# Optimization experiments

Measured on AMD Instinct MI355X. Metric: run time of the kernel, lower is better.

The kernel has to match this reference:

```python
import jax, jax.numpy as jnp
import numpy as np

SIG = [1, 1, 1, 1, -1]  # Cl(4,1)
NVEC = 5
GA = 1 << NVEC  # 32


def _build_gp_table():
    # Cayley table for the geometric product on blades indexed by bitmask.
    G = np.zeros((GA, GA, GA), np.float32)
    for a in range(GA):
        for b in range(GA):
            s = 0
            t = a >> 1
            while t:
                s += bin(t & b).count('1')
                t >>= 1
            sign = -1.0 if (s & 1) else 1.0
            common = a & b
            for i in range(NVEC):
                if (common >> i) & 1:
                    sign *= SIG[i]
            G[a, b, a ^ b] = sign
    return G

GP_TABLE = jnp.asarray(_build_gp_table())


def geometric_product(x, y):
    return jnp.einsum('...i,...j,ijk->...k', x, y, GP_TABLE)


def manifold_norm(x):
    # normalize each multivector onto the unit sphere in R^32
    return x / (jnp.linalg.norm(x, axis=-1, keepdims=True) + 1e-6)


def versor_linear(x, W, b):
    # channel mixing shared across multivector components: x [..., in, ga]
    return jnp.einsum('...ig,oi->...og', x, W) + b


def layer_norm2d(x, w, b):
    # LayerNorm over last two dims [D, ga] jointly
    mu = jnp.mean(x, axis=(-2, -1), keepdims=True)
    var = jnp.var(x, axis=(-2, -1), keepdims=True)
    return (x - mu) / jnp.sqrt(var + 1e-5) * w + b


def attention(x, Wq, bq, Wk, bk, Wv, bv, Wo, bo, n_heads):
    B, S, D, G = x.shape
    dh = D // n_heads
    q = versor_linear(x, Wq, bq).reshape(B, S, n_heads, dh, G)
    k = versor_linear(x, Wk, bk).reshape(B, S, n_heads, dh, G)
    v = versor_linear(x, Wv, bv).reshape(B, S, n_heads, dh, G)
    scale = 1.0 / np.sqrt(dh * G).astype(np.float32)
    scores = jnp.einsum('bshdg,bthdg->bhst', q, k) * scale
    probs = jax.nn.softmax(scores, axis=-1)
    o = jnp.einsum('bhst,bthdg->bshdg', probs, v).reshape(B, S, D, G)
    return versor_linear(o, Wo, bo)


N_HEADS = 8


def forward(x, Wq, bq, Wk, bk, Wv, bv, Wo, bo, ln1_w, ln1_b, ln2_w, ln2_b,
            gamma1, gamma2, W1, b1, W2, b2, Wr, br, Wc, bc):
    L = Wq.shape[0]
    for l in range(L):
        h = attention(layer_norm2d(x, ln1_w[l], ln1_b[l]),
                      Wq[l], bq[l], Wk[l], bk[l], Wv[l], bv[l], Wo[l], bo[l], N_HEADS)
        x = manifold_norm(x + gamma1[l] * h)
        m = versor_linear(layer_norm2d(x, ln2_w[l], ln2_b[l]), W1[l], b1[l])
        m = versor_linear(jnp.tanh(m), W2[l], b2[l])
        x = manifold_norm(x + gamma2[l] * m)
    # RecursiveRotorAccumulator: log(S)-step inclusive scan of rotors
    delta = versor_linear(x, Wr, br)
    rot = 0.5 * delta
    rot = rot.at[..., 0].add(1.0)
    rot = manifold_norm(rot)
    S = x.shape[1]
    step = 1
    while step < S:
        left = rot[:, :-step]
        right = rot[:, step:]
        comb = manifold_norm(geometric_product(right, left))
        rot = jnp.concatenate([rot[:, :step], comb], axis=1)
        step *= 2
    pooled = rot[:, -1]  # [B, D, ga]
    logits = pooled.reshape(pooled.shape[0], -1) @ Wc.T + bc
    return logits


def setup_inputs() -> dict:
    key = jax.random.key(0)
    B, S, D, G, L, NC = 8, 256, 64, GA, 4, 1000
    E = 4 * D  # expansion hidden
    ks = jax.random.split(key, 16)
    sd = 0.02
    inp = {
        'x': jax.random.normal(ks[0], (B, S, D, G), jnp.float32),
        'Wq': jax.random.normal(ks[1], (L, D, D), jnp.float32) * sd,
        'bq': jnp.zeros((L, D, G), jnp.float32),
        'Wk': jax.random.normal(ks[2], (L, D, D), jnp.float32) * sd,
        'bk': jnp.zeros((L, D, G), jnp.float32),
        'Wv': jax.random.normal(ks[3], (L, D, D), jnp.float32) * sd,
        'bv': jnp.zeros((L, D, G), jnp.float32),
        'Wo': jax.random.normal(ks[4], (L, D, D), jnp.float32) * sd,
        'bo': jnp.zeros((L, D, G), jnp.float32),
        'ln1_w': jnp.ones((L, D, G), jnp.float32),
        'ln1_b': jnp.zeros((L, D, G), jnp.float32),
        'ln2_w': jnp.ones((L, D, G), jnp.float32),
        'ln2_b': jnp.zeros((L, D, G), jnp.float32),
        'gamma1': 1e-5 * jnp.ones((L, D, G), jnp.float32),
        'gamma2': 1e-5 * jnp.ones((L, D, G), jnp.float32),
        'W1': jax.random.normal(ks[5], (L, E, D), jnp.float32) * sd,
        'b1': jnp.zeros((L, E, G), jnp.float32),
        'W2': jax.random.normal(ks[6], (L, D, E), jnp.float32) * sd,
        'b2': jnp.zeros((L, D, G), jnp.float32),
        'Wr': jax.random.normal(ks[7], (D, D), jnp.float32) * sd,
        'br': jnp.zeros((D, G), jnp.float32),
        'Wc': jax.random.normal(ks[8], (NC, D * G), jnp.float32) * sd,
        'bc': jnp.zeros((NC,), jnp.float32),
    }
    return inp


def reference(x, Wq, bq, Wk, bk, Wv, bv, Wo, bo, ln1_w, ln1_b, ln2_w, ln2_b,
              gamma1, gamma2, W1, b1, W2, b2, Wr, br, Wc, bc):
    return forward(x, Wq, bq, Wk, bk, Wv, bv, Wo, bo, ln1_w, ln1_b, ln2_w, ln2_b,
                   gamma1, gamma2, W1, b1, W2, b2, Wr, br, Wc, bc)
```

## Files before the change

kernel.cpp:

```cpp
#include <hip/hip_runtime.h>
#include <hip/hip_bf16.h>

constexpr int kB  = 8;
constexpr int kS  = 256;
constexpr int kD  = 64;
constexpr int kG  = 32;
constexpr int kE  = 256;
constexpr int kNH = 8;
constexpr int kHD = 256;
constexpr int kDG = kD * kG;
constexpr int kT  = kB * kS;
constexpr int kNC = 1000;

using bf16x8 = __attribute__((ext_vector_type(8))) short;
using f32x4  = __attribute__((ext_vector_type(4))) float;

__device__ __forceinline__ short f2bf(float f) {
    unsigned u = __float_as_uint(f);
    unsigned r = (u + 0x7FFFu + ((u >> 16) & 1u)) >> 16;
    return (short)r;
}

__device__ __forceinline__ float tanh_fast(float x) {
    float a = fabsf(x);
    float e = __expf(-2.f * a);
    float d = 1.f + e;
    float r = __builtin_amdgcn_rcpf(d);
    r = r * (2.f - d * r);
    float t = (1.f - e) * r;
    return copysignf(t, x);
}

__global__ __launch_bounds__(256) void cvtw_kernel(
    const float* __restrict__ Wq, const float* __restrict__ Wk,
    const float* __restrict__ Wv, const float* __restrict__ Wo,
    const float* __restrict__ W1, const float* __restrict__ W2,
    unsigned short* __restrict__ dst) {
    int idx = (blockIdx.x * 256 + threadIdx.x) * 4;
    const float* src; int off;
    if      (idx <  16384) { src = Wq; off = 0; }
    else if (idx <  32768) { src = Wk; off = 16384; }
    else if (idx <  49152) { src = Wv; off = 32768; }
    else if (idx <  65536) { src = Wo; off = 49152; }
    else if (idx < 131072) { src = W1; off = 65536; }
    else                   { src = W2; off = 131072; }
    const float4 v = *(const float4*)(src + (idx - off));
    *(short4*)&dst[idx] = make_short4(f2bf(v.x), f2bf(v.y), f2bf(v.z), f2bf(v.w));
}

__global__ __launch_bounds__(256) void prep_tr_kernel(
    const float* __restrict__ bq, const float* __restrict__ bk,
    const float* __restrict__ bv, const float* __restrict__ bo,
    const float* __restrict__ b2, const float* __restrict__ gm1,
    const float* __restrict__ gm2, const float* __restrict__ ln2w,
    const float* __restrict__ ln2b, const float* __restrict__ ln1w,
    const float* __restrict__ ln1b, const float* __restrict__ b1,
    float* __restrict__ dst) {
    __shared__ float lt[32 * 257];
    const int a = blockIdx.x >> 2, l = blockIdx.x & 3;
    const float* srcs[12] = {bq, bk, bv, bo, b2, gm1, gm2, ln2w, ln2b, ln1w, ln1b, b1};
    const int R  = (a == 11) ? 256 : 64;
    const int sh = (a == 11) ? 8 : 6;
    const float* src = srcs[a] + (size_t)l * R * 32;
    float* out = dst + a * 8192 + l * R * 32;
    const int tid = threadIdx.x;
    for (int j = tid; j < R * 32; j += 256) lt[(j & 31) * (R + 1) + (j >> 5)] = src[j];
    __syncthreads();
    for (int k = tid; k < R * 32; k += 256) {
        int g = k >> sh, r = k & (R - 1);
        out[k] = lt[g * (R + 1) + r];
    }
}

__global__ __launch_bounds__(256) void ln_kernel(const float* __restrict__ Xin,
                                                 const float* __restrict__ w,
                                                 const float* __restrict__ b,
                                                 unsigned short* __restrict__ A,
                                                 float* __restrict__ XT) {
    int t = blockIdx.x, tid = threadIdx.x;
    const float* xp = Xin + (size_t)t * kDG;
    __shared__ float r1[256], r2[256];
    __shared__ short st[32 * 72];
    __shared__ float xf[32 * 68];
    float v[8], s = 0.f, ss = 0.f;
#pragma unroll
    for (int j = 0; j < 8; j++) {
        float x = xp[tid + j * 256];
        v[j] = x; s += x; ss += x * x;
        int jj = tid + j * 256;
        xf[(jj & 31) * 68 + (jj >> 5)] = x;
    }
    r1[tid] = s; r2[tid] = ss; __syncthreads();
    for (int o = 128; o > 0; o >>= 1) {
        if (tid < o) { r1[tid] += r1[tid + o]; r2[tid] += r2[tid + o]; }
        __syncthreads();
    }
    float mean = r1[0] * (1.f / kDG);
    float var  = r2[0] * (1.f / kDG) - mean * mean;
    float rstd = rsqrtf(var + 1e-5f);
#pragma unroll
    for (int j = 0; j < 8; j++) {
        int jj = tid + j * 256;
        float val = (v[j] - mean) * rstd * w[jj] + b[jj];
        st[(jj & 31) * 72 + (jj >> 5)] = f2bf(val);
    }
    __syncthreads();
    bf16x8 ov = *(const bf16x8*)&st[(tid >> 3) * 72 + (tid & 7) * 8];
    *(bf16x8*)&A[(size_t)t * kDG + tid * 8] = ov;
    const int row = tid >> 3, col = (tid & 7) * 8;
    float* xo = XT + (size_t)t * kDG + tid * 8;
    *(float4*)(xo + 0) = *(const float4*)&xf[row * 68 + col + 0];
    *(float4*)(xo + 4) = *(const float4*)&xf[row * 68 + col + 4];
}

template<int MT>
__device__ __forceinline__ void epiT(
    const f32x4 (&acc)[MT][2], const float* __restrict__ bT,
    float* __restrict__ XTp, const float* __restrict__ gT,
    int l16, int quad, int obase,
    float& s, float& ss, float (&xv)[MT][2][4]) {
    s = 0.f; ss = 0.f;
#pragma unroll
    for (int mt = 0; mt < MT; ++mt) {
        int o0 = obase + mt * 16 + quad * 4;
        float vv[2][4];
#pragma unroll
        for (int nt = 0; nt < 2; ++nt) {
            int g = nt * 16 + l16;
            const float4 b4 = *(const float4*)&bT[g * kD + o0];
            const float4 g4 = *(const float4*)&gT[g * kD + o0];
            const float4 xi = *(const float4*)&XTp[g * kD + o0];
#pragma unroll
            for (int r = 0; r < 4; ++r)
                vv[nt][r] = (&xi.x)[r] + (&g4.x)[r] * (acc[mt][nt][r] + (&b4.x)[r]);
        }
        float rn[4];
#pragma unroll
        for (int r = 0; r < 4; ++r) {
            float sq = vv[0][r] * vv[0][r] + vv[1][r] * vv[1][r];
#pragma unroll
            for (int off = 1; off < 16; off <<= 1) sq += __shfl_xor(sq, off, 64);
            rn[r] = 1.f / (sqrtf(sq) + 1e-6f);
        }
#pragma unroll
        for (int nt = 0; nt < 2; ++nt) {
            int g = nt * 16 + l16;
            float4 xo;
#pragma unroll
            for (int r = 0; r < 4; ++r) {
                float x = vv[nt][r] * rn[r];
                (&xo.x)[r] = x; xv[mt][nt][r] = x;
                s += x; ss = fmaf(x, x, ss);
            }
            *(float4*)&XTp[g * kD + o0] = xo;
        }
    }
}

template<int MT>
__device__ __forceinline__ void lnT(
    const float (&xv)[MT][2][4], const float* __restrict__ lwT,
    const float* __restrict__ lbT, unsigned short* __restrict__ Aoutp,
    int l16, int quad, int obase, float mean, float rstd) {
#pragma unroll
    for (int mt = 0; mt < MT; ++mt)
#pragma unroll
        for (int nt = 0; nt < 2; ++nt) {
            int g = nt * 16 + l16;
            int o0 = obase + mt * 16 + quad * 4;
            const float4 w4 = *(const float4*)&lwT[g * kD + o0];
            const float4 b4 = *(const float4*)&lbT[g * kD + o0];
            short4 s4;
#pragma unroll
            for (int r = 0; r < 4; ++r)
                (&s4.x)[r] = f2bf((xv[mt][nt][r] - mean) * rstd * (&w4.x)[r] + (&b4.x)[r]);
            *(short4*)&Aoutp[g * kD + o0] = s4;
        }
}

__global__ __launch_bounds__(256) void vlinT_kernel(const float* __restrict__ XT,
                                                    const float* __restrict__ W,
                                                    const float* __restrict__ bias,
                                                    float* __restrict__ OutT) {
    __shared__ float sx[32 * 65];
    __shared__ float sw[kD * kD];
    int t = blockIdx.x, tid = threadIdx.x;
    const float* xp = XT + (size_t)t * kDG;
    for (int j = tid; j < kDG; j += 256) sx[(j >> 6) * 65 + (j & 63)] = xp[j];
    for (int j = tid; j < kD * kD; j += 256) sw[j] = W[j];
    __syncthreads();
    int g = tid & 31, ob = tid >> 5;
    int b = t >> 8, s = t & 255;
    float* op = OutT + ((size_t)b * kD * kS + s) * kG;
    for (int o = ob; o < kD; o += 8) {
        float acc = bias[o * kG + g];
        const float* wr = sw + o * kD;
#pragma unroll
        for (int i = 0; i < kD; i++) acc += wr[i] * sx[g * 65 + i];
        op[(size_t)o * kS * kG + g] = acc;
    }
}

template<bool DO_LN>
__global__ __launch_bounds__(128, 4) void mlp_fused_kernel(
    const unsigned short* __restrict__ A,
    const unsigned short* __restrict__ W1h,
    const float* __restrict__ b1T,
    const unsigned short* __restrict__ W2h,
    const float* __restrict__ b2T,
    float* __restrict__ XT, const float* __restrict__ gmT,
    const float* __restrict__ lwT, const float* __restrict__ lbT,
    unsigned short* __restrict__ Aout) {
    constexpr int MS = 264;
    __shared__ short sM[32 * MS];
    __shared__ float sred[4];
    const int tid = threadIdx.x;
    const int w = tid >> 6, lane = tid & 63;
    const int l16 = lane & 15, quad = lane >> 4;
    const int tok = blockIdx.x;

    const unsigned short* xp = A + (size_t)tok * kDG;
    bf16x8 bfr[2][2];
#pragma unroll
    for (int c = 0; c < 2; ++c)
#pragma unroll
        for (int nt = 0; nt < 2; ++nt)
            bfr[c][nt] = *(const bf16x8*)&xp[(nt * 16 + l16) * kD + c * 32 + quad * 8];

    f32x4 acc[8][2];
#pragma unroll
    for (int mt = 0; mt < 8; ++mt)
#pragma unroll
        for (int nt = 0; nt < 2; ++nt) acc[mt][nt] = (f32x4){0.f, 0.f, 0.f, 0.f};

#pragma unroll
    for (int mt = 0; mt < 8; ++mt)
#pragma unroll
        for (int c = 0; c < 2; ++c) {
            bf16x8 afr = *(const bf16x8*)&W1h[((w * 8 + mt) * 16 + l16) * kD + c * 32 + quad * 8];
#pragma unroll
            for (int nt = 0; nt < 2; ++nt)
                acc[mt][nt] = __builtin_amdgcn_mfma_f32_16x16x32_bf16(afr, bfr[c][nt], acc[mt][nt], 0, 0, 0);
        }

#pragma unroll
    for (int mt = 0; mt < 8; ++mt)
#pragma unroll
        for (int nt = 0; nt < 2; ++nt) {
            int g = nt * 16 + l16;
            int e0 = (w * 8 + mt) * 16 + quad * 4;
            const float4 b4 = *(const float4*)&b1T[g * kE + e0];
            short4 s4;
#pragma unroll
            for (int r = 0; r < 4; ++r)
                (&s4.x)[r] = f2bf(tanh_fast(acc[mt][nt][r] + (&b4.x)[r]));
            *(short4*)&sM[g * MS + e0] = s4;
        }
    __syncthreads();

    f32x4 acc2[2][2];
#pragma unroll
    for (int mt = 0; mt < 2; ++mt)
#pragma unroll
        for (int nt = 0; nt < 2; ++nt) acc2[mt][nt] = (f32x4){0.f, 0.f, 0.f, 0.f};

#pragma unroll
    for (int c = 0; c < 8; ++c) {
        bf16x8 bq[2];
#pragma unroll
        for (int nt = 0; nt < 2; ++nt)
            bq[nt] = *(const bf16x8*)&sM[(nt * 16 + l16) * MS + c * 32 + quad * 8];
#pragma unroll
        for (int mt = 0; mt < 2; ++mt) {
            bf16x8 afr = *(const bf16x8*)&W2h[(w * 32 + mt * 16 + l16) * kE + c * 32 + quad * 8];
#pragma unroll
            for (int nt = 0; nt < 2; ++nt)
                acc2[mt][nt] = __builtin_amdgcn_mfma_f32_16x16x32_bf16(afr, bq[nt], acc2[mt][nt], 0, 0, 0);
        }
    }

    const size_t tb = (size_t)tok * kDG;
    float xv[2][2][4]; float s, ss;
    epiT<2>(acc2, b2T, XT + tb, gmT, l16, quad, w * 32, s, ss, xv);
    if (DO_LN) {
#pragma unroll
        for (int off = 1; off < 64; off <<= 1) {
            s += __shfl_xor(s, off, 64); ss += __shfl_xor(ss, off, 64);
        }
        if (lane == 0) { sred[w] = s; sred[2 + w] = ss; }
        __syncthreads();
        float st = sred[0] + sred[1], sst = sred[2] + sred[3];
        float mean = st * (1.f / kDG);
        float var  = sst * (1.f / kDG) - mean * mean;
        float rstd = rsqrtf(var + 1e-5f);
        lnT<2>(xv, lwT, lbT, Aout + tb, l16, quad, w * 32, mean, rstd);
    }
}

__global__ __launch_bounds__(256, 3) void gemmWo_fused_kernel(
    const unsigned short* __restrict__ X, const unsigned short* __restrict__ Wh,
    const float* __restrict__ bT,
    float* __restrict__ XT, const float* __restrict__ gmT,
    const float* __restrict__ lwT, const float* __restrict__ lbT,
    unsigned short* __restrict__ Aout) {
    constexpr int WS = 64 + 8;
    __shared__ short sW[64 * WS];

    const int tid = threadIdx.x, wave = tid >> 6, lane = tid & 63;
    const int l16 = lane & 15, quad = lane >> 4;
    const int tok = blockIdx.x * 4 + wave;

    for (int j = tid * 8; j < 64 * 64; j += 2048) {
        int o = j >> 6, i = j & 63;
        *(bf16x8*)&sW[o * WS + i] = *(const bf16x8*)(Wh + j);
    }

    const unsigned short* xp = X + (size_t)tok * kDG;
    bf16x8 bfr[2][2];
#pragma unroll
    for (int c = 0; c < 2; ++c)
#pragma unroll
        for (int nt = 0; nt < 2; ++nt)
            bfr[c][nt] = *(const bf16x8*)&xp[(nt * 16 + l16) * kD + c * 32 + quad * 8];
    __syncthreads();

    f32x4 acc[4][2];
#pragma unroll
    for (int mt = 0; mt < 4; ++mt)
#pragma unroll
        for (int nt = 0; nt < 2; ++nt) acc[mt][nt] = (f32x4){0.f, 0.f, 0.f, 0.f};

#pragma unroll
    for (int mt = 0; mt < 4; ++mt)
#pragma unroll
        for (int c = 0; c < 2; ++c) {
            bf16x8 afr = *(const bf16x8*)&sW[(mt * 16 + l16) * WS + c * 32 + quad * 8];
#pragma unroll
            for (int nt = 0; nt < 2; ++nt)
                acc[mt][nt] = __builtin_amdgcn_mfma_f32_16x16x32_bf16(afr, bfr[c][nt], acc[mt][nt], 0, 0, 0);
        }

    const size_t tb = (size_t)tok * kDG;
    float xv[4][2][4]; float s, ss;
    epiT<4>(acc, bT, XT + tb, gmT, l16, quad, 0, s, ss, xv);
#pragma unroll
    for (int off = 1; off < 64; off <<= 1) {
        s += __shfl_xor(s, off, 64); ss += __shfl_xor(ss, off, 64);
    }
    float mean = s * (1.f / kDG);
    float var  = ss * (1.f / kDG) - mean * mean;
    float rstd = rsqrtf(var + 1e-5f);
    lnT<4>(xv, lwT, lbT, Aout + tb, l16, quad, 0, mean, rstd);
}

__global__ __launch_bounds__(256, 3) void gemm_qkv_kernel(
    const unsigned short* __restrict__ X,
    const unsigned short* __restrict__ Wqh, const unsigned short* __restrict__ Wkh,
    const unsigned short* __restrict__ Wvh,
    const float* __restrict__ bqT, const float* __restrict__ bkT, const float* __restrict__ bvT,
    unsigned short* __restrict__ Q, unsigned short* __restrict__ K, unsigned short* __restrict__ V) {
    constexpr int WS = 64 + 8;
    __shared__ short sW[3 * 64 * WS];

    const int tid = threadIdx.x, wave = tid >> 6, lane = tid & 63;
    const int l16 = lane & 15, quad = lane >> 4;
    const int tok = blockIdx.x * 4 + wave;

    const unsigned short* Wp[3] = {Wqh, Wkh, Wvh};
#pragma unroll
    for (int w = 0; w < 3; ++w)
        for (int j = tid * 8; j < 64 * 64; j += 2048) {
            int o = j >> 6, i = j & 63;
            *(bf16x8*)&sW[w * 64 * WS + o * WS + i] = *(const bf16x8*)(Wp[w] + j);
        }

    const unsigned short* xp = X + (size_t)tok * kDG;
    bf16x8 bfr[2][2];
#pragma unroll
    for (int c = 0; c < 2; ++c)
#pragma unroll
        for (int nt = 0; nt < 2; ++nt)
            bfr[c][nt] = *(const bf16x8*)&xp[(nt * 16 + l16) * kD + c * 32 + quad * 8];
    __syncthreads();

    f32x4 acc[3][4][2];
#pragma unroll
    for (int w = 0; w < 3; ++w)
#pragma unroll
        for (int mt = 0; mt < 4; ++mt)
#pragma unroll
            for (int nt = 0; nt < 2; ++nt) acc[w][mt][nt] = (f32x4){0.f, 0.f, 0.f, 0.f};

#pragma unroll
    for (int w = 0; w < 3; ++w)
#pragma unroll
        for (int mt = 0; mt < 4; ++mt)
#pragma unroll
            for (int c = 0; c < 2; ++c) {
                bf16x8 afr = *(const bf16x8*)&sW[w * 64 * WS + (mt * 16 + l16) * WS + c * 32 + quad * 8];
#pragma unroll
                for (int nt = 0; nt < 2; ++nt)
                    acc[w][mt][nt] = __builtin_amdgcn_mfma_f32_16x16x32_bf16(afr, bfr[c][nt], acc[w][mt][nt], 0, 0, 0);
            }

    unsigned short* Op[3] = {Q, K, V};
    const float* Bp[3] = {bqT, bkT, bvT};
#pragma unroll
    for (int w = 0; w < 3; ++w) {
        unsigned short* op = Op[w] + (size_t)tok * kDG;
#pragma unroll
        for (int mt = 0; mt < 4; ++mt)
#pragma unroll
            for (int nt = 0; nt < 2; ++nt) {
                int g = nt * 16 + l16;
                int o0 = mt * 16 + quad * 4;
                const float4 b4 = *(const float4*)&Bp[w][g * kD + o0];
#pragma unroll
                for (int r = 0; r < 4; ++r)
                    op[(o0 + r) * kG + g] = (unsigned short)f2bf(acc[w][mt][nt][r] + (&b4.x)[r]);
            }
    }
}

constexpr int QSTR = 264;
constexpr int VSTR = 40;

__global__ __launch_bounds__(256) void attn_mfma_kernel(const unsigned short* __restrict__ Q,
                                                        const unsigned short* __restrict__ K,
                                                        const unsigned short* __restrict__ V,
                                                        unsigned short* __restrict__ O) {
    __shared__ short sQ[64 * QSTR];
    __shared__ short sKV[2][256 * VSTR];

    const int qt = blockIdx.x, h = blockIdx.y, b = blockIdx.z;
    const int tid = threadIdx.x;
    const int wave = tid >> 6, lane = tid & 63;
    const int l16 = lane & 15, quad = lane >> 4;

    const size_t bh = (size_t)b * kS * kDG + (size_t)h * kHD;

#pragma unroll
    for (int it = 0; it < 8; ++it) {
        int j = it * 2048 + tid * 8;
        int row = j >> 8, col = j & 255;
        *(bf16x8*)&sQ[row * QSTR + col] =
            *(const bf16x8*)(Q + bh + (size_t)(qt * 64 + row) * kDG + col);
    }
#pragma unroll
    for (int it = 0; it < 4; ++it) {
        int j = it * 2048 + tid * 8;
        int row = j >> 8, col = j & 255;
        *(bf16x8*)&sKV[0][row * QSTR + col] =
            *(const bf16x8*)(K + bh + (size_t)row * kDG + col);
    }
    __syncthreads();

    bf16x8 afrag[8];
    {
        int row = wave * 16 + l16;
#pragma unroll
        for (int c = 0; c < 8; ++c)
            afrag[c] = *(const bf16x8*)&sQ[row * QSTR + c * 32 + quad * 8];
    }

    f32x4 acc[16];
#pragma unroll
    for (int i = 0; i < 16; ++i) acc[i] = (f32x4){0.f, 0.f, 0.f, 0.f};

    for (int kt = 0; kt < 8; ++kt) {
        bf16x8 kpre[4];
        if (kt < 7) {
#pragma unroll
            for (int it = 0; it < 4; ++it) {
                int j = it * 2048 + tid * 8;
                int row = j >> 8, col = j & 255;
                kpre[it] = *(const bf16x8*)(K + bh + (size_t)((kt + 1) * 32 + row) * kDG + col);
            }
        }
        const short* kb = sKV[kt & 1];
#pragma unroll
        for (int nt = 0; nt < 2; ++nt) {
            int key = nt * 16 + l16;
            f32x4 a = acc[kt * 2 + nt];
#pragma unroll
            for (int c = 0; c < 8; ++c) {
                bf16x8 bfrag = *(const bf16x8*)&kb[key * QSTR + c * 32 + quad * 8];
                a = __builtin_amdgcn_mfma_f32_16x16x32_bf16(afrag[c], bfrag, a, 0, 0, 0);
            }
            acc[kt * 2 + nt] = a;
        }
        if (kt < 7) {
            short* nb = sKV[(kt + 1) & 1];
#pragma unroll
            for (int it = 0; it < 4; ++it) {
                int j = it * 2048 + tid * 8;
                int row = j >> 8, col = j & 255;
                *(bf16x8*)&nb[row * QSTR + col] = kpre[it];
            }
            __syncthreads();
        }
    }

    float inv[4];
#pragma unroll
    for (int r = 0; r < 4; ++r) {
        float m = -1e30f;
#pragma unroll
        for (int t = 0; t < 16; ++t) m = fmaxf(m, acc[t][r]);
#pragma unroll
        for (int off = 1; off < 16; off <<= 1) m = fmaxf(m, __shfl_xor(m, off, 16));
        float s = 0.f;
#pragma unroll
        for (int t = 0; t < 16; ++t) {
            float p = __expf((acc[t][r] - m) * 0.0625f);
            acc[t][r] = p; s += p;
        }
#pragma unroll
        for (int off = 1; off < 16; off <<= 1) s += __shfl_xor(s, off, 16);
        inv[r] = 1.f / s;
    }

#pragma unroll
    for (int t = 0; t < 16; ++t)
#pragma unroll
        for (int r = 0; r < 4; ++r)
            sQ[(wave * 16 + quad * 4 + r) * QSTR + t * 16 + l16] = f2bf(acc[t][r]);

    {
        int kb = tid >> 5;
#pragma unroll
        for (int it = 0; it < 2; ++it) {
            int db = (tid & 31) + it * 32;
            short4 vr[4];
#pragma unroll
            for (int r = 0; r < 4; ++r)
                vr[r] = *(const short4*)(V + bh + (size_t)(kb * 4 + r) * kDG + db * 4);
#pragma unroll
            for (int i = 0; i < 4; ++i) {
                short4 p = make_short4((&vr[0].x)[i], (&vr[1].x)[i],
                                       (&vr[2].x)[i], (&vr[3].x)[i]);
                *(short4*)&sKV[0][(db * 4 + i) * VSTR + kb * 4] = p;
            }
        }
    }
    __syncthreads();

    f32x4 oacc[16];
#pragma unroll
    for (int i = 0; i < 16; ++i) oacc[i] = (f32x4){0.f, 0.f, 0.f, 0.f};

    for (int vt = 0; vt < 8; ++vt) {
        short4 vpre[8];
        if (vt < 7) {
            int kb = tid >> 5;
#pragma unroll
            for (int it = 0; it < 2; ++it) {
                int db = (tid & 31) + it * 32;
#pragma unroll
                for (int r = 0; r < 4; ++r)
                    vpre[it * 4 + r] = *(const short4*)(V + bh + (size_t)((vt + 1) * 32 + kb * 4 + r) * kDG + db * 4);
            }
        }
        const short* vb = sKV[vt & 1];
        bf16x8 pfrag = *(const bf16x8*)&sQ[(wave * 16 + l16) * QSTR + vt * 32 + quad * 8];
#pragma unroll
        for (int dt = 0; dt < 16; ++dt) {
            bf16x8 vfrag = *(const bf16x8*)&vb[(dt * 16 + l16) * VSTR + quad * 8];
            oacc[dt] = __builtin_amdgcn_mfma_f32_16x16x32_bf16(pfrag, vfrag, oacc[dt], 0, 0, 0);
        }
        if (vt < 7) {
            short* nb = sKV[(vt + 1) & 1];
            int kb = tid >> 5;
#pragma unroll
            for (int it = 0; it < 2; ++it) {
                int db = (tid & 31) + it * 32;
#pragma unroll
                for (int i = 0; i < 4; ++i) {
                    short4 p = make_short4((&vpre[it * 4 + 0].x)[i], (&vpre[it * 4 + 1].x)[i],
                                           (&vpre[it * 4 + 2].x)[i], (&vpre[it * 4 + 3].x)[i]);
                    *(short4*)&nb[(db * 4 + i) * VSTR + kb * 4] = p;
                }
            }
            __syncthreads();
        }
    }

    {
        const size_t ob = (size_t)(b * kS + qt * 64 + wave * 16 + quad * 4) * kDG + h * 8;
#pragma unroll
        for (int gg = 0; gg < 2; ++gg) {
            int g = gg * 16 + l16;
#pragma unroll
            for (int r = 0; r < 4; ++r) {
                bf16x8 pk;
#pragma unroll
                for (int k = 0; k < 8; ++k)
                    pk[k] = f2bf(oacc[k * 2 + gg][r] * inv[r]);
                *(bf16x8*)&O[ob + (size_t)r * kDG + g * kD] = pk;
            }
        }
    }
}

constexpr int pc_ce(unsigned v) { int c = 0; while (v) { c += v & 1; v >>= 1; } return c; }
constexpr unsigned gp_mask_ce(int a) {
    unsigned m = 0;
    for (int c = 0; c < 32; ++c) {
        int b = a ^ c;
        int s = (a & b) >> 4;
        for (int t = a >> 1; t; t >>= 1) s += pc_ce(t & b);
        if (s & 1) m |= (1u << c);
    }
    return m;
}

template<int A>
__device__ __forceinline__ void gp_term(const float* x, const float* y, float* acc) {
    constexpr unsigned m = gp_mask_ce(A);
    const float xa = x[A], nxa = -xa;
#pragma unroll
    for (int c = 0; c < 32; ++c)
        acc[c] = fmaf(((m >> c) & 1u) ? nxa : xa, y[A ^ c], acc[c]);
}

__device__ __forceinline__ void gp_mn_t(const float* x, const float* y, float* out) {
    float acc[32];
#pragma unroll
    for (int c = 0; c < 32; ++c) acc[c] = 0.f;
    gp_term<0>(x, y, acc);  gp_term<1>(x, y, acc);  gp_term<2>(x, y, acc);  gp_term<3>(x, y, acc);
    gp_term<4>(x, y, acc);  gp_term<5>(x, y, acc);  gp_term<6>(x, y, acc);  gp_term<7>(x, y, acc);
    gp_term<8>(x, y, acc);  gp_term<9>(x, y, acc);  gp_term<10>(x, y, acc); gp_term<11>(x, y, acc);
    gp_term<12>(x, y, acc); gp_term<13>(x, y, acc); gp_term<14>(x, y, acc); gp_term<15>(x, y, acc);
    gp_term<16>(x, y, acc); gp_term<17>(x, y, acc); gp_term<18>(x, y, acc); gp_term<19>(x, y, acc);
    gp_term<20>(x, y, acc); gp_term<21>(x, y, acc); gp_term<22>(x, y, acc); gp_term<23>(x, y, acc);
    gp_term<24>(x, y, acc); gp_term<25>(x, y, acc); gp_term<26>(x, y, acc); gp_term<27>(x, y, acc);
    gp_term<28>(x, y, acc); gp_term<29>(x, y, acc); gp_term<30>(x, y, acc); gp_term<31>(x, y, acc);
    float ss = 0.f;
#pragma unroll
    for (int c = 0; c < 32; ++c) ss = fmaf(acc[c], acc[c], ss);
    float r = 1.f / (sqrtf(ss) + 1e-6f);
#pragma unroll
    for (int c = 0; c < 32; ++c) out[c] = acc[c] * r;
}

__device__ __forceinline__ void leaf_load(const float* base, float* v) {
#pragma unroll
    for (int i = 0; i < 8; ++i) {
        const float4 f = *(const float4*)(base + i * 4);
        v[i * 4 + 0] = 0.5f * f.x; v[i * 4 + 1] = 0.5f * f.y;
        v[i * 4 + 2] = 0.5f * f.z; v[i * 4 + 3] = 0.5f * f.w;
    }
    v[0] += 1.f;
    float ss = 0.f;
#pragma unroll
    for (int c = 0; c < 32; ++c) ss = fmaf(v[c], v[c], ss);
    float r = 1.f / (sqrtf(ss) + 1e-6f);
#pragma unroll
    for (int c = 0; c < 32; ++c) v[c] *= r;
}

__global__ __launch_bounds__(256) void scanreg_kernel(const float* __restrict__ DT,
                                                      float* __restrict__ pooled) {
    const int wave = threadIdx.x >> 6, lane = threadIdx.x & 63;
    const int seq = blockIdx.x * 4 + wave;
    const float* base = DT + ((size_t)seq * kS + lane * 4) * kG;

    float R[32], Y[32], P[32], Xa[32], Yb[32];

    leaf_load(base, R);
    for (int j = 1; j < 4; ++j) {
        leaf_load(base + j * kG, Y);
        gp_mn_t(Y, R, R);
    }

    for (int step = 1; step < 64; step <<= 1) {
        const bool up = lane & step;
#pragma unroll
        for (int c = 0; c < 32; ++c) P[c] = __shfl_xor(R[c], step, 64);
#pragma unroll
        for (int c = 0; c < 32; ++c) {
            Xa[c] = up ? R[c] : P[c];
            Yb[c] = up ? P[c] : R[c];
        }
        gp_mn_t(Xa, Yb, R);
    }

    if (lane == 0) {
        float* op = pooled + (size_t)seq * kG;
#pragma unroll
        for (int i = 0; i < 8; ++i)
            *(float4*)(op + i * 4) = make_float4(R[i * 4], R[i * 4 + 1], R[i * 4 + 2], R[i * 4 + 3]);
    }
}

__global__ __launch_bounds__(256) void cls2_kernel(const float* __restrict__ P,
                                                   const float* __restrict__ Wc,
                                                   const float* __restrict__ bc,
                                                   float* __restrict__ out) {
    __shared__ float sp[kB * kDG];
    const int tid = threadIdx.x, wave = tid >> 6, lane = tid & 63;
    for (int j = tid * 4; j < kB * kDG; j += 1024)
        *(float4*)&sp[j] = *(const float4*)(P + j);
    __syncthreads();

    const int c = blockIdx.x * 4 + wave;
    const float* w = Wc + (size_t)c * kDG;
    float acc[kB];
#pragma unroll
    for (int b = 0; b < kB; ++b) acc[b] = 0.f;
#pragma unroll
    for (int cc = 0; cc < 8; ++cc) {
        const float4 w4 = *(const float4*)(w + cc * 256 + lane * 4);
#pragma unroll
        for (int b = 0; b < kB; ++b) {
            const float4 p4 = *(const float4*)&sp[b * kDG + cc * 256 + lane * 4];
            acc[b] += w4.x * p4.x + w4.y * p4.y + w4.z * p4.z + w4.w * p4.w;
        }
    }
#pragma unroll
    for (int b = 0; b < kB; ++b)
#pragma unroll
        for (int off = 32; off > 0; off >>= 1) acc[b] += __shfl_xor(acc[b], off, 64);
    if (lane == 0) {
        float bias = bc[c];
#pragma unroll
        for (int b = 0; b < kB; ++b) out[b * kNC + c] = acc[b] + bias;
    }
}

extern "C" void kernel_launch(void* const* d_in, const int* in_sizes, int n_in,
                              void* d_out, int out_size, void* d_ws, size_t ws_size,
                              hipStream_t stream) {
    const float* x_in = (const float*)d_in[0];
    const float* Wq   = (const float*)d_in[1];
    const float* bq   = (const float*)d_in[2];
    const float* Wk   = (const float*)d_in[3];
    const float* bk   = (const float*)d_in[4];
    const float* Wv   = (const float*)d_in[5];
    const float* bv   = (const float*)d_in[6];
    const float* Wo   = (const float*)d_in[7];
    const float* bo   = (const float*)d_in[8];
    const float* ln1w = (const float*)d_in[9];
    const float* ln1b = (const float*)d_in[10];
    const float* ln2w = (const float*)d_in[11];
    const float* ln2b = (const float*)d_in[12];
    const float* gm1  = (const float*)d_in[13];
    const float* gm2  = (const float*)d_in[14];
    const float* W1   = (const float*)d_in[15];
    const float* b1   = (const float*)d_in[16];
    const float* W2   = (const float*)d_in[17];
    const float* b2   = (const float*)d_in[18];
    const float* Wr   = (const float*)d_in[19];
    const float* br   = (const float*)d_in[20];
    const float* Wc   = (const float*)d_in[21];
    const float* bc   = (const float*)d_in[22];

    const size_t NEL = (size_t)kT * kDG;
    float* F  = (float*)d_ws;
    float* XT = F;
    unsigned short* Abf = (unsigned short*)(F + NEL);
    unsigned short* Qh = (unsigned short*)(F + 2 * NEL);
    unsigned short* Kh = (unsigned short*)(F + 3 * NEL);
    unsigned short* Vh = (unsigned short*)(F + 4 * NEL);
    unsigned short* Wb = (unsigned short*)(F + 5 * NEL);
    float* PT = F + 3 * NEL + NEL / 2;
    float* pooled = F + 2 * NEL;
    float* DT = F + NEL;

    cvtw_kernel<<<192, 256, 0, stream>>>(Wq, Wk, Wv, Wo, W1, W2, Wb);
    prep_tr_kernel<<<48, 256, 0, stream>>>(bq, bk, bv, bo, b2, gm1, gm2,
                                           ln2w, ln2b, ln1w, ln1b, b1, PT);
    unsigned short* Wqh = Wb;
    unsigned short* Wkh = Wb + 16384;
    unsigned short* Wvh = Wb + 32768;
    unsigned short* Woh = Wb + 49152;
    unsigned short* W1h = Wb + 65536;
    unsigned short* W2h = Wb + 131072;

    auto bqT   = [&](int l) { return PT + 0     + l * 2048; };
    auto bkT   = [&](int l) { return PT + 8192  + l * 2048; };
    auto bvT   = [&](int l) { return PT + 16384 + l * 2048; };
    auto boT   = [&](int l) { return PT + 24576 + l * 2048; };
    auto b2T   = [&](int l) { return PT + 32768 + l * 2048; };
    auto gm1T  = [&](int l) { return PT + 40960 + l * 2048; };
    auto gm2T  = [&](int l) { return PT + 49152 + l * 2048; };
    auto ln2wT = [&](int l) { return PT + 57344 + l * 2048; };
    auto ln2bT = [&](int l) { return PT + 65536 + l * 2048; };
    auto ln1wT = [&](int l) { return PT + 73728 + l * 2048; };
    auto ln1bT = [&](int l) { return PT + 81920 + l * 2048; };
    auto b1T   = [&](int l) { return PT + 90112 + l * 8192; };

    ln_kernel<<<kT, 256, 0, stream>>>(x_in, ln1w, ln1b, Abf, XT);

    for (int l = 0; l < 4; l++) {
        gemm_qkv_kernel<<<kT / 4, 256, 0, stream>>>(Abf,
            Wqh + l * 4096, Wkh + l * 4096, Wvh + l * 4096,
            bqT(l), bkT(l), bvT(l), Qh, Kh, Vh);
        attn_mfma_kernel<<<dim3(4, kNH, kB), 256, 0, stream>>>(Qh, Kh, Vh, Abf);
        gemmWo_fused_kernel<<<kT / 4, 256, 0, stream>>>(Abf, Woh + l * 4096, boT(l),
            XT, gm1T(l), ln2wT(l), ln2bT(l), Abf);
        if (l < 3)
            mlp_fused_kernel<true><<<kT, 128, 0, stream>>>(Abf,
                W1h + l * 16384, b1T(l), W2h + l * 16384, b2T(l),
                XT, gm2T(l), ln1wT(l + 1), ln1bT(l + 1), Abf);
        else
            mlp_fused_kernel<false><<<kT, 128, 0, stream>>>(Abf,
                W1h + l * 16384, b1T(l), W2h + l * 16384, b2T(l),
                XT, gm2T(l), nullptr, nullptr, nullptr);
    }

    vlinT_kernel<<<kT, 256, 0, stream>>>(XT, Wr, br, DT);
    scanreg_kernel<<<kB * kD / 4, 256, 0, stream>>>(DT, pooled);
    cls2_kernel<<<kNC / 4, 256, 0, stream>>>(pooled, Wc, bc, (float*)d_out);
}
```

Baseline: 552.8 us.

## Fuse Wo projection, MLP, and next-layer QKV into one per-token kernel

Merges the Wo GEMM with its residual/normalize/LN2 epilogue, the MLP, and the next layer's LN1 plus QKV projection into a single per-token kernel. Intermediate activations stay in registers and shared memory instead of going through global memory. This removes two kernel launches per layer and the associated global reads and writes. In exchange, Wo and QKV weights are now read directly from global/L2 per block rather than staged in shared memory, and QKV stores are scattered 2-byte writes, which may raise register pressure and store traffic.

```diff
diff --git a/kernel.cpp b/kernel.cpp
--- a/kernel.cpp
+++ b/kernel.cpp
@@ -113,71 +113,6 @@
     *(float4*)(xo + 4) = *(const float4*)&xf[row * 68 + col + 4];
 }
 
-template<int MT>
-__device__ __forceinline__ void epiT(
-    const f32x4 (&acc)[MT][2], const float* __restrict__ bT,
-    float* __restrict__ XTp, const float* __restrict__ gT,
-    int l16, int quad, int obase,
-    float& s, float& ss, float (&xv)[MT][2][4]) {
-    s = 0.f; ss = 0.f;
-#pragma unroll
-    for (int mt = 0; mt < MT; ++mt) {
-        int o0 = obase + mt * 16 + quad * 4;
-        float vv[2][4];
-#pragma unroll
-        for (int nt = 0; nt < 2; ++nt) {
-            int g = nt * 16 + l16;
-            const float4 b4 = *(const float4*)&bT[g * kD + o0];
-            const float4 g4 = *(const float4*)&gT[g * kD + o0];
-            const float4 xi = *(const float4*)&XTp[g * kD + o0];
-#pragma unroll
-            for (int r = 0; r < 4; ++r)
-                vv[nt][r] = (&xi.x)[r] + (&g4.x)[r] * (acc[mt][nt][r] + (&b4.x)[r]);
-        }
-        float rn[4];
-#pragma unroll
-        for (int r = 0; r < 4; ++r) {
-            float sq = vv[0][r] * vv[0][r] + vv[1][r] * vv[1][r];
-#pragma unroll
-            for (int off = 1; off < 16; off <<= 1) sq += __shfl_xor(sq, off, 64);
-            rn[r] = 1.f / (sqrtf(sq) + 1e-6f);
-        }
-#pragma unroll
-        for (int nt = 0; nt < 2; ++nt) {
-            int g = nt * 16 + l16;
-            float4 xo;
-#pragma unroll
-            for (int r = 0; r < 4; ++r) {
-                float x = vv[nt][r] * rn[r];
-                (&xo.x)[r] = x; xv[mt][nt][r] = x;
-                s += x; ss = fmaf(x, x, ss);
-            }
-            *(float4*)&XTp[g * kD + o0] = xo;
-        }
-    }
-}
-
-template<int MT>
-__device__ __forceinline__ void lnT(
-    const float (&xv)[MT][2][4], const float* __restrict__ lwT,
-    const float* __restrict__ lbT, unsigned short* __restrict__ Aoutp,
-    int l16, int quad, int obase, float mean, float rstd) {
-#pragma unroll
-    for (int mt = 0; mt < MT; ++mt)
-#pragma unroll
-        for (int nt = 0; nt < 2; ++nt) {
-            int g = nt * 16 + l16;
-            int o0 = obase + mt * 16 + quad * 4;
-            const float4 w4 = *(const float4*)&lwT[g * kD + o0];
-            const float4 b4 = *(const float4*)&lbT[g * kD + o0];
-            short4 s4;
-#pragma unroll
-            for (int r = 0; r < 4; ++r)
-                (&s4.x)[r] = f2bf((xv[mt][nt][r] - mean) * rstd * (&w4.x)[r] + (&b4.x)[r]);
-            *(short4*)&Aoutp[g * kD + o0] = s4;
-        }
-}
-
 __global__ __launch_bounds__(256) void vlinT_kernel(const float* __restrict__ XT,
                                                     const float* __restrict__ W,
                                                     const float* __restrict__ bias,
@@ -201,88 +136,89 @@
     }
 }
 
-template<bool DO_LN>
-__global__ __launch_bounds__(128, 4) void mlp_fused_kernel(
-    const unsigned short* __restrict__ A,
-    const unsigned short* __restrict__ W1h,
-    const float* __restrict__ b1T,
-    const unsigned short* __restrict__ W2h,
-    const float* __restrict__ b2T,
-    float* __restrict__ XT, const float* __restrict__ gmT,
-    const float* __restrict__ lwT, const float* __restrict__ lbT,
-    unsigned short* __restrict__ Aout) {
+template<bool LAST>
+__global__ __launch_bounds__(128, 4) void mega_kernel(
+    const unsigned short* __restrict__ O,
+    const unsigned short* __restrict__ Woh, const float* __restrict__ boT,
+    const float* __restrict__ gm1T,
+    const float* __restrict__ ln2wT, const float* __restrict__ ln2bT,
+    const unsigned short* __restrict__ W1h, const float* __restrict__ b1T,
+    const unsigned short* __restrict__ W2h, const float* __restrict__ b2T,
+    const float* __restrict__ gm2T,
+    const float* __restrict__ ln1wT, const float* __restrict__ ln1bT,
+    float* __restrict__ XT,
+    const unsigned short* __restrict__ Wqh, const unsigned short* __restrict__ Wkh,
+    const unsigned short* __restrict__ Wvh,
+    const float* __restrict__ bqT, const float* __restrict__ bkT,
+    const float* __restrict__ bvT,
+    unsigned short* __restrict__ Q, unsigned short* __restrict__ K,
+    unsigned short* __restrict__ V) {
+    constexpr int AS = 72;
     constexpr int MS = 264;
+    __shared__ short sA[32 * AS];
     __shared__ short sM[32 * MS];
     __shared__ float sred[4];
+
     const int tid = threadIdx.x;
     const int w = tid >> 6, lane = tid & 63;
     const int l16 = lane & 15, quad = lane >> 4;
     const int tok = blockIdx.x;
-
-    const unsigned short* xp = A + (size_t)tok * kDG;
-    bf16x8 bfr[2][2];
-#pragma unroll
-    for (int c = 0; c < 2; ++c)
-#pragma unroll
-        for (int nt = 0; nt < 2; ++nt)
-            bfr[c][nt] = *(const bf16x8*)&xp[(nt * 16 + l16) * kD + c * 32 + quad * 8];
-
-    f32x4 acc[8][2];
-#pragma unroll
-    for (int mt = 0; mt < 8; ++mt)
-#pragma unroll
-        for (int nt = 0; nt < 2; ++nt) acc[mt][nt] = (f32x4){0.f, 0.f, 0.f, 0.f};
-
-#pragma unroll
-    for (int mt = 0; mt < 8; ++mt)
-#pragma unroll
-        for (int c = 0; c < 2; ++c) {
-            bf16x8 afr = *(const bf16x8*)&W1h[((w * 8 + mt) * 16 + l16) * kD + c * 32 + quad * 8];
+    const size_t tb = (size_t)tok * kDG;
+
+    float xv[2][2][4];
+    {
+        const unsigned short* xp = O + tb;
+        bf16x8 bfr[2][2];
+#pragma unroll
+        for (int c = 0; c < 2; ++c)
 #pragma unroll
             for (int nt = 0; nt < 2; ++nt)
-                acc[mt][nt] = __builtin_amdgcn_mfma_f32_16x16x32_bf16(afr, bfr[c][nt], acc[mt][nt], 0, 0, 0);
-        }
-
-#pragma unroll
-    for (int mt = 0; mt < 8; ++mt)
-#pragma unroll
-        for (int nt = 0; nt < 2; ++nt) {
-            int g = nt * 16 + l16;
-            int e0 = (w * 8 + mt) * 16 + quad * 4;
-            const float4 b4 = *(const float4*)&b1T[g * kE + e0];
-            short4 s4;
-#pragma unroll
-            for (int r = 0; r < 4; ++r)
-                (&s4.x)[r] = f2bf(tanh_fast(acc[mt][nt][r] + (&b4.x)[r]));
-            *(short4*)&sM[g * MS + e0] = s4;
-        }
-    __syncthreads();
-
-    f32x4 acc2[2][2];
-#pragma unroll
-    for (int mt = 0; mt < 2; ++mt)
-#pragma unroll
-        for (int nt = 0; nt < 2; ++nt) acc2[mt][nt] = (f32x4){0.f, 0.f, 0.f, 0.f};
-
-#pragma unroll
-    for (int c = 0; c < 8; ++c) {
-        bf16x8 bq[2];
-#pragma unroll
-        for (int nt = 0; nt < 2; ++nt)
-            bq[nt] = *(const bf16x8*)&sM[(nt * 16 + l16) * MS + c * 32 + quad * 8];
+                bfr[c][nt] = *(const bf16x8*)&xp[(nt * 16 + l16) * kD + c * 32 + quad * 8];
+
+        f32x4 accW[2][2];
+#pragma unroll
+        for (int mt = 0; mt < 2; ++mt)
+#pragma unroll
+            for (int nt = 0; nt < 2; ++nt) accW[mt][nt] = (f32x4){0.f, 0.f, 0.f, 0.f};
+#pragma unroll
+        for (int mt = 0; mt < 2; ++mt)
+#pragma unroll
+            for (int c = 0; c < 2; ++c) {
+                bf16x8 afr = *(const bf16x8*)&Woh[(w * 32 + mt * 16 + l16) * kD + c * 32 + quad * 8];
+#pragma unroll
+                for (int nt = 0; nt < 2; ++nt)
+                    accW[mt][nt] = __builtin_amdgcn_mfma_f32_16x16x32_bf16(afr, bfr[c][nt], accW[mt][nt], 0, 0, 0);
+            }
+
+        float s = 0.f, ss = 0.f;
 #pragma unroll
         for (int mt = 0; mt < 2; ++mt) {
-            bf16x8 afr = *(const bf16x8*)&W2h[(w * 32 + mt * 16 + l16) * kE + c * 32 + quad * 8];
-#pragma unroll
-            for (int nt = 0; nt < 2; ++nt)
-                acc2[mt][nt] = __builtin_amdgcn_mfma_f32_16x16x32_bf16(afr, bq[nt], acc2[mt][nt], 0, 0, 0);
-        }
-    }
-
-    const size_t tb = (size_t)tok * kDG;
-    float xv[2][2][4]; float s, ss;
-    epiT<2>(acc2, b2T, XT + tb, gmT, l16, quad, w * 32, s, ss, xv);
-    if (DO_LN) {
+            int o0 = w * 32 + mt * 16 + quad * 4;
+            float vv[2][4];
+#pragma unroll
+            for (int nt = 0; nt < 2; ++nt) {
+                int g = nt * 16 + l16;
+                const float4 b4 = *(const float4*)&boT[g * kD + o0];
+                const float4 g4 = *(const float4*)&gm1T[g * kD + o0];
+                const float4 xi = *(const float4*)&XT[tb + g * kD + o0];
+#pragma unroll
+                for (int r = 0; r < 4; ++r)
+                    vv[nt][r] = (&xi.x)[r] + (&g4.x)[r] * (accW[mt][nt][r] + (&b4.x)[r]);
+            }
+#pragma unroll
+            for (int r = 0; r < 4; ++r) {
+                float sq = vv[0][r] * vv[0][r] + vv[1][r] * vv[1][r];
+#pragma unroll
+                for (int off = 1; off < 16; off <<= 1) sq += __shfl_xor(sq, off, 64);
+                float rn = 1.f / (sqrtf(sq) + 1e-6f);
+#pragma unroll
+                for (int nt = 0; nt < 2; ++nt) {
+                    float x = vv[nt][r] * rn;
+                    xv[mt][nt][r] = x;
+                    s += x; ss = fmaf(x, x, ss);
+                }
+            }
+        }
 #pragma unroll
         for (int off = 1; off < 64; off <<= 1) {
             s += __shfl_xor(s, off, 64); ss += __shfl_xor(ss, off, 64);
@@ -293,64 +229,189 @@
         float mean = st * (1.f / kDG);
         float var  = sst * (1.f / kDG) - mean * mean;
         float rstd = rsqrtf(var + 1e-5f);
-        lnT<2>(xv, lwT, lbT, Aout + tb, l16, quad, w * 32, mean, rstd);
-    }
-}
-
-__global__ __launch_bounds__(256, 3) void gemmWo_fused_kernel(
-    const unsigned short* __restrict__ X, const unsigned short* __restrict__ Wh,
-    const float* __restrict__ bT,
-    float* __restrict__ XT, const float* __restrict__ gmT,
-    const float* __restrict__ lwT, const float* __restrict__ lbT,
-    unsigned short* __restrict__ Aout) {
-    constexpr int WS = 64 + 8;
-    __shared__ short sW[64 * WS];
-
-    const int tid = threadIdx.x, wave = tid >> 6, lane = tid & 63;
-    const int l16 = lane & 15, quad = lane >> 4;
-    const int tok = blockIdx.x * 4 + wave;
-
-    for (int j = tid * 8; j < 64 * 64; j += 2048) {
-        int o = j >> 6, i = j & 63;
-        *(bf16x8*)&sW[o * WS + i] = *(const bf16x8*)(Wh + j);
-    }
-
-    const unsigned short* xp = X + (size_t)tok * kDG;
-    bf16x8 bfr[2][2];
-#pragma unroll
-    for (int c = 0; c < 2; ++c)
+#pragma unroll
+        for (int mt = 0; mt < 2; ++mt)
+#pragma unroll
+            for (int nt = 0; nt < 2; ++nt) {
+                int g = nt * 16 + l16;
+                int o0 = w * 32 + mt * 16 + quad * 4;
+                const float4 w4 = *(const float4*)&ln2wT[g * kD + o0];
+                const float4 b4 = *(const float4*)&ln2bT[g * kD + o0];
+                short4 s4;
+#pragma unroll
+                for (int r = 0; r < 4; ++r)
+                    (&s4.x)[r] = f2bf((xv[mt][nt][r] - mean) * rstd * (&w4.x)[r] + (&b4.x)[r]);
+                *(short4*)&sA[g * AS + o0] = s4;
+            }
+    }
+    __syncthreads();
+
+    {
+        bf16x8 afrA[2][2];
+#pragma unroll
+        for (int c = 0; c < 2; ++c)
+#pragma unroll
+            for (int nt = 0; nt < 2; ++nt)
+                afrA[c][nt] = *(const bf16x8*)&sA[(nt * 16 + l16) * AS + c * 32 + quad * 8];
+
+        f32x4 acc1[8][2];
+#pragma unroll
+        for (int mt = 0; mt < 8; ++mt)
+#pragma unroll
+            for (int nt = 0; nt < 2; ++nt) acc1[mt][nt] = (f32x4){0.f, 0.f, 0.f, 0.f};
+#pragma unroll
+        for (int mt = 0; mt < 8; ++mt)
+#pragma unroll
+            for (int c = 0; c < 2; ++c) {
+                bf16x8 afr = *(const bf16x8*)&W1h[((w * 8 + mt) * 16 + l16) * kD + c * 32 + quad * 8];
+#pragma unroll
+                for (int nt = 0; nt < 2; ++nt)
+                    acc1[mt][nt] = __builtin_amdgcn_mfma_f32_16x16x32_bf16(afr, afrA[c][nt], acc1[mt][nt], 0, 0, 0);
+            }
+#pragma unroll
+        for (int mt = 0; mt < 8; ++mt)
+#pragma unroll
+            for (int nt = 0; nt < 2; ++nt) {
+                int g = nt * 16 + l16;
+                int e0 = (w * 8 + mt) * 16 + quad * 4;
+                const float4 b4 = *(const float4*)&b1T[g * kE + e0];
+                short4 s4;
+#pragma unroll
+                for (int r = 0; r < 4; ++r)
+                    (&s4.x)[r] = f2bf(tanh_fast(acc1[mt][nt][r] + (&b4.x)[r]));
+                *(short4*)&sM[g * MS + e0] = s4;
+            }
+    }
+    __syncthreads();
+
+    f32x4 acc2[2][2];
+#pragma unroll
+    for (int mt = 0; mt < 2; ++mt)
+#pragma unroll
+        for (int nt = 0; nt < 2; ++nt) acc2[mt][nt] = (f32x4){0.f, 0.f, 0.f, 0.f};
+#pragma unroll
+    for (int c = 0; c < 8; ++c) {
+        bf16x8 bq[2];
 #pragma unroll
         for (int nt = 0; nt < 2; ++nt)
-            bfr[c][nt] = *(const bf16x8*)&xp[(nt * 16 + l16) * kD + c * 32 + quad * 8];
-    __syncthreads();
-
-    f32x4 acc[4][2];
-#pragma unroll
-    for (int mt = 0; mt < 4; ++mt)
-#pragma unroll
-        for (int nt = 0; nt < 2; ++nt) acc[mt][nt] = (f32x4){0.f, 0.f, 0.f, 0.f};
-
-#pragma unroll
-    for (int mt = 0; mt < 4; ++mt)
-#pragma unroll
-        for (int c = 0; c < 2; ++c) {
-            bf16x8 afr = *(const bf16x8*)&sW[(mt * 16 + l16) * WS + c * 32 + quad * 8];
+            bq[nt] = *(const bf16x8*)&sM[(nt * 16 + l16) * MS + c * 32 + quad * 8];
+#pragma unroll
+        for (int mt = 0; mt < 2; ++mt) {
+            bf16x8 afr = *(const bf16x8*)&W2h[(w * 32 + mt * 16 + l16) * kE + c * 32 + quad * 8];
 #pragma unroll
             for (int nt = 0; nt < 2; ++nt)
-                acc[mt][nt] = __builtin_amdgcn_mfma_f32_16x16x32_bf16(afr, bfr[c][nt], acc[mt][nt], 0, 0, 0);
-        }
-
-    const size_t tb = (size_t)tok * kDG;
-    float xv[4][2][4]; float s, ss;
-    epiT<4>(acc, bT, XT + tb, gmT, l16, quad, 0, s, ss, xv);
+                acc2[mt][nt] = __builtin_amdgcn_mfma_f32_16x16x32_bf16(afr, bq[nt], acc2[mt][nt], 0, 0, 0);
+        }
+    }
+
+    float yv[2][2][4];
+    float s2 = 0.f, ss2 = 0.f;
+#pragma unroll
+    for (int mt = 0; mt < 2; ++mt) {
+        int o0 = w * 32 + mt * 16 + quad * 4;
+        float vv[2][4];
+#pragma unroll
+        for (int nt = 0; nt < 2; ++nt) {
+            int g = nt * 16 + l16;
+            const float4 b4 = *(const float4*)&b2T[g * kD + o0];
+            const float4 g4 = *(const float4*)&gm2T[g * kD + o0];
+#pragma unroll
+            for (int r = 0; r < 4; ++r)
+                vv[nt][r] = xv[mt][nt][r] + (&g4.x)[r] * (acc2[mt][nt][r] + (&b4.x)[r]);
+        }
+#pragma unroll
+        for (int r = 0; r < 4; ++r) {
+            float sq = vv[0][r] * vv[0][r] + vv[1][r] * vv[1][r];
+#pragma unroll
+            for (int off = 1; off < 16; off <<= 1) sq += __shfl_xor(sq, off, 64);
+            float rn = 1.f / (sqrtf(sq) + 1e-6f);
+#pragma unroll
+            for (int nt = 0; nt < 2; ++nt) {
+                float x = vv[nt][r] * rn;
+                yv[mt][nt][r] = x;
+                s2 += x; ss2 = fmaf(x, x, ss2);
+            }
+        }
+#pragma unroll
+        for (int nt = 0; nt < 2; ++nt) {
+            int g = nt * 16 + l16;
+            float4 xo;
+#pragma unroll
+            for (int r = 0; r < 4; ++r) (&xo.x)[r] = yv[mt][nt][r];
+            *(float4*)&XT[tb + g * kD + o0] = xo;
+        }
+    }
+    if constexpr (LAST) return;
+
 #pragma unroll
     for (int off = 1; off < 64; off <<= 1) {
-        s += __shfl_xor(s, off, 64); ss += __shfl_xor(ss, off, 64);
-    }
-    float mean = s * (1.f / kDG);
-    float var  = ss * (1.f / kDG) - mean * mean;
-    float rstd = rsqrtf(var + 1e-5f);
-    lnT<4>(xv, lwT, lbT, Aout + tb, l16, quad, 0, mean, rstd);
+        s2 += __shfl_xor(s2, off, 64); ss2 += __shfl_xor(ss2, off, 64);
+    }
+    if (lane == 0) { sred[w] = s2; sred[2 + w] = ss2; }
+    __syncthreads();
+    {
+        float st = sred[0] + sred[1], sst = sred[2] + sred[3];
+        float mean = st * (1.f / kDG);
+        float var  = sst * (1.f / kDG) - mean * mean;
+        float rstd = rsqrtf(var + 1e-5f);
+#pragma unroll
+        for (int mt = 0; mt < 2; ++mt)
+#pragma unroll
+            for (int nt = 0; nt < 2; ++nt) {
+                int g = nt * 16 + l16;
+                int o0 = w * 32 + mt * 16 + quad * 4;
+                const float4 w4 = *(const float4*)&ln1wT[g * kD + o0];
+                const float4 b4 = *(const float4*)&ln1bT[g * kD + o0];
+                short4 s4;
+#pragma unroll
+                for (int r = 0; r < 4; ++r)
+                    (&s4.x)[r] = f2bf((yv[mt][nt][r] - mean) * rstd * (&w4.x)[r] + (&b4.x)[r]);
+                *(short4*)&sA[g * AS + o0] = s4;
+            }
+    }
+    __syncthreads();
+
+    {
+        bf16x8 afrA[2][2];
+#pragma unroll
+        for (int c = 0; c < 2; ++c)
+#pragma unroll
+            for (int nt = 0; nt < 2; ++nt)
+                afrA[c][nt] = *(const bf16x8*)&sA[(nt * 16 + l16) * AS + c * 32 + quad * 8];
+
+        const unsigned short* Wp[3] = {Wqh, Wkh, Wvh};
+        const float* Bp[3] = {bqT, bkT, bvT};
+        unsigned short* Op[3] = {Q, K, V};
+#pragma unroll
+        for (int m = 0; m < 3; ++m) {
+            f32x4 acc3[2][2];
+#pragma unroll
+            for (int mt = 0; mt < 2; ++mt)
+#pragma unroll
+                for (int nt = 0; nt < 2; ++nt) acc3[mt][nt] = (f32x4){0.f, 0.f, 0.f, 0.f};
+#pragma unroll
+            for (int mt = 0; mt < 2; ++mt)
+#pragma unroll
+                for (int c = 0; c < 2; ++c) {
+                    bf16x8 afr = *(const bf16x8*)&Wp[m][(w * 32 + mt * 16 + l16) * kD + c * 32 + quad * 8];
+#pragma unroll
+                    for (int nt = 0; nt < 2; ++nt)
+                        acc3[mt][nt] = __builtin_amdgcn_mfma_f32_16x16x32_bf16(afr, afrA[c][nt], acc3[mt][nt], 0, 0, 0);
+                }
+            unsigned short* op = Op[m] + tb;
+#pragma unroll
+            for (int mt = 0; mt < 2; ++mt)
+#pragma unroll
+                for (int nt = 0; nt < 2; ++nt) {
+                    int g = nt * 16 + l16;
+                    int o0 = w * 32 + mt * 16 + quad * 4;
+                    const float4 b4 = *(const float4*)&Bp[m][g * kD + o0];
+#pragma unroll
+                    for (int r = 0; r < 4; ++r)
+                        op[(o0 + r) * kG + g] = (unsigned short)f2bf(acc3[mt][nt][r] + (&b4.x)[r]);
+                }
+        }
+    }
 }
 
 __global__ __launch_bounds__(256, 3) void gemm_qkv_kernel(
@@ -791,22 +852,25 @@
     auto b1T   = [&](int l) { return PT + 90112 + l * 8192; };
 
     ln_kernel<<<kT, 256, 0, stream>>>(x_in, ln1w, ln1b, Abf, XT);
+    gemm_qkv_kernel<<<kT / 4, 256, 0, stream>>>(Abf,
+        Wqh, Wkh, Wvh, bqT(0), bkT(0), bvT(0), Qh, Kh, Vh);
 
     for (int l = 0; l < 4; l++) {
-        gemm_qkv_kernel<<<kT / 4, 256, 0, stream>>>(Abf,
-            Wqh + l * 4096, Wkh + l * 4096, Wvh + l * 4096,
-            bqT(l), bkT(l), bvT(l), Qh, Kh, Vh);
         attn_mfma_kernel<<<dim3(4, kNH, kB), 256, 0, stream>>>(Qh, Kh, Vh, Abf);
-        gemmWo_fused_kernel<<<kT / 4, 256, 0, stream>>>(Abf, Woh + l * 4096, boT(l),
-            XT, gm1T(l), ln2wT(l), ln2bT(l), Abf);
         if (l < 3)
-            mlp_fused_kernel<true><<<kT, 128, 0, stream>>>(Abf,
-                W1h + l * 16384, b1T(l), W2h + l * 16384, b2T(l),
-                XT, gm2T(l), ln1wT(l + 1), ln1bT(l + 1), Abf);
+            mega_kernel<false><<<kT, 128, 0, stream>>>(Abf,
+                Woh + l * 4096, boT(l), gm1T(l), ln2wT(l), ln2bT(l),
+                W1h + l * 16384, b1T(l), W2h + l * 16384, b2T(l), gm2T(l),
+                ln1wT(l + 1), ln1bT(l + 1), XT,
+                Wqh + (l + 1) * 4096, Wkh + (l + 1) * 4096, Wvh + (l + 1) * 4096,
+                bqT(l + 1), bkT(l + 1), bvT(l + 1), Qh, Kh, Vh);
         else
-            mlp_fused_kernel<false><<<kT, 128, 0, stream>>>(Abf,
-                W1h + l * 16384, b1T(l), W2h + l * 16384, b2T(l),
-                XT, gm2T(l), nullptr, nullptr, nullptr);
+            mega_kernel<true><<<kT, 128, 0, stream>>>(Abf,
+                Woh + l * 4096, boT(l), gm1T(l), ln2wT(l), ln2bT(l),
+                W1h + l * 16384, b1T(l), W2h + l * 16384, b2T(l), gm2T(l),
+                nullptr, nullptr, XT,
+                nullptr, nullptr, nullptr, nullptr, nullptr, nullptr,
+                nullptr, nullptr, nullptr);
     }
 
     vlinT_kernel<<<kT, 256, 0, stream>>>(XT, Wr, br, DT);
```

Result: faster. 521.1 us (-5.7%).
